# Kernel optimization log

Hardware: AMD Instinct MI355X
Metric: run time of the kernel (lower is better)

The kernel has to match this reference:

```python
import jax, jax.numpy as jnp
import numpy as np

B, T, DIN, E, H, P = 8, 2048, 256, 256, 4, 8
HD = E // H


def _xavier(key, out_dim, in_dim):
    lim = float(np.sqrt(6.0 / (in_dim + out_dim)))
    return jax.random.uniform(key, (out_dim, in_dim), jnp.float32, -lim, lim)


def setup_inputs() -> dict:
    key = jax.random.key(0)
    ks = jax.random.split(key, 9)
    return {
        "x": jax.random.normal(ks[0], (B, T, DIN), jnp.float32),
        "w_in": _xavier(ks[1], E, DIN), "b_in": jnp.zeros((E,), jnp.float32),
        # MHA in-projections (torch packs qkv; xavier over packed [3E,E] approximated per-slice)
        "w_q": _xavier(ks[2], E, E), "b_q": jnp.zeros((E,), jnp.float32),
        "w_k": _xavier(ks[3], E, E), "b_k": jnp.zeros((E,), jnp.float32),
        "w_v": _xavier(ks[4], E, E), "b_v": jnp.zeros((E,), jnp.float32),
        "w_o": _xavier(ks[5], E, E), "b_o": jnp.zeros((E,), jnp.float32),
        "w_bd": _xavier(ks[6], 1, E), "b_bd": jnp.zeros((1,), jnp.float32),
        "w_pr": _xavier(ks[7], E, E), "b_pr": jnp.zeros((E,), jnp.float32),
    }


def reference(x, w_in, b_in, w_q, b_q, w_k, b_k, w_v, b_v, w_o, b_o, w_bd, b_bd, w_pr, b_pr):
    b, t, _ = x.shape
    h = x @ w_in.T + b_in                                   # [B,T,E]
    # self-attention (batch_first MHA, eval mode -> dropout is identity)
    q = (h @ w_q.T + b_q).reshape(b, t, H, HD)
    k = (h @ w_k.T + b_k).reshape(b, t, H, HD)
    v = (h @ w_v.T + b_v).reshape(b, t, H, HD)
    scale = 1.0 / np.sqrt(HD).astype(np.float32)
    scores = jnp.einsum("bqhd,bkhd->bhqk", q * scale, k)   # [B,H,T,T]
    attn = jax.nn.softmax(scores, axis=-1)
    ao = jnp.einsum("bhqk,bkhd->bqhd", attn, v).reshape(b, t, E)
    ao = ao @ w_o.T + b_o
    # boundary scoring -> dynamic patch ids
    bs = jax.nn.sigmoid(ao @ w_bd.T + b_bd)[..., 0]         # [B,T]
    cum = jnp.cumsum(bs, axis=1)
    normalized = cum / jnp.maximum(cum[:, -1:], 1e-6)
    pid = jnp.minimum((normalized * P).astype(jnp.int32), P - 1)  # [B,T]
    # mean-pool h into P dynamic patches (scatter_add + counts, via one-hot segment matmul)
    oh = jax.nn.one_hot(pid, P, dtype=h.dtype)              # [B,T,P]
    patch_emb = jnp.einsum("btp,btd->bpd", oh, h)           # [B,P,E]
    counts = oh.sum(axis=1)[..., None]                      # [B,P,1]
    patch_emb = patch_emb / jnp.maximum(counts, 1.0)
    return patch_emb @ w_pr.T + b_pr                        # [B,P,E]
```

## Files before the change

### kernel.cpp

```cpp
#include <hip/hip_runtime.h>
#include <cstddef>

#define NB 8
#define NT 2048
#define NE 256
#define NH 4
#define ND 64
#define NP 8

typedef short bf16x8 __attribute__((ext_vector_type(8)));
typedef float f32x4 __attribute__((ext_vector_type(4)));
typedef float f32x16 __attribute__((ext_vector_type(16)));

__device__ __forceinline__ unsigned short f2bf(float f) {
  unsigned u = __builtin_bit_cast(unsigned, f);
  u += 0x7fffu + ((u >> 16) & 1u);
  return (unsigned short)(u >> 16);
}
__device__ __forceinline__ float bf2f(unsigned short h) {
  unsigned u = ((unsigned)h) << 16;
  return __builtin_bit_cast(float, u);
}
__device__ __forceinline__ void split2(float a, float b, unsigned& hi, unsigned& lo) {
  const unsigned short ha = f2bf(a), hb = f2bf(b);
  hi = (unsigned)ha | ((unsigned)hb << 16);
  const unsigned short la = f2bf(a - bf2f(ha));
  const unsigned short lb = f2bf(b - bf2f(hb));
  lo = (unsigned)la | ((unsigned)lb << 16);
}
__device__ __forceinline__ void gld16(const void* g, void* l) {
  __builtin_amdgcn_global_load_lds((const __attribute__((address_space(1))) unsigned*)g,
                                   (__attribute__((address_space(3))) unsigned*)l, 16, 0, 0);
}

#define QSC 0.180336880111120419f

__global__ __launch_bounds__(256) void setup1_kernel(
    const float* __restrict__ w_o, const float* __restrict__ b_o,
    const float* __restrict__ w_bd, const float* __restrict__ b_bd,
    const float* __restrict__ w_v, const float* __restrict__ b_v,
    float* __restrict__ uvbuf, float* __restrict__ consts)
{
  __shared__ float wbd_s[NE];
  __shared__ float u_s[NE];
  const int tid = threadIdx.x;
  wbd_s[tid] = w_bd[tid];
  __syncthreads();
  float a = 0.f;
  for (int j = 0; j < NE; ++j) a = fmaf(wbd_s[j], w_o[j * NE + tid], a);
  u_s[tid] = a;
  __syncthreads();
  #pragma unroll
  for (int hh = 0; hh < NH; ++hh) {
    float a2 = 0.f;
    for (int d = 0; d < ND; ++d)
      a2 = fmaf(u_s[hh * ND + d], w_v[(size_t)(hh * ND + d) * NE + tid], a2);
    uvbuf[hh * NE + tid] = a2;
  }
  if (tid == 0) {
    float cc = 0.f;
    for (int j = 0; j < NE; ++j) cc = fmaf(wbd_s[j], b_o[j], cc);
    consts[0] = cc + b_bd[0];
  }
  if (tid >= 8 && tid < 12) {
    const int hh = tid - 8;
    float cv = 0.f;
    for (int d = 0; d < ND; ++d) cv = fmaf(u_s[hh * ND + d], b_v[hh * ND + d], cv);
    consts[1 + hh] = cv;
  }
}

__global__ __launch_bounds__(256) void setup2_kernel(
    const float* __restrict__ w_in, const float* __restrict__ w_q,
    const float* __restrict__ w_k, const float* __restrict__ b_in,
    const float* __restrict__ b_q, const float* __restrict__ b_k,
    const float* __restrict__ uvbuf, const float* __restrict__ consts,
    unsigned short* __restrict__ wfhi, unsigned short* __restrict__ wflo,
    float* __restrict__ bias_f, float* __restrict__ psum)
{
  __shared__ float row_s[256];
  __shared__ float red[256];
  const int b = blockIdx.x, tid = threadIdx.x;
  if (b == 832) {
    for (int i = tid; i < NB * NP * NE; i += 256) psum[i] = 0.f;
    return;
  }
  float v = 0.f, bias = 0.f;
  if (b < 256) {
    v = w_in[(size_t)b * 256 + tid];
    bias = b_in[b];
  } else if (b < 772) {
    const float* wrow = (b < 512) ? (w_q + (size_t)(b - 256) * 256)
                      : (b < 768) ? (w_k + (size_t)(b - 512) * 256)
                                  : (uvbuf + (size_t)(b - 768) * 256);
    row_s[tid] = wrow[tid];
    __syncthreads();
    float acc = 0.f;
    for (int e = 0; e < 256; ++e) acc = fmaf(row_s[e], w_in[(size_t)e * 256 + tid], acc);
    v = acc;
    red[tid] = row_s[tid] * b_in[tid];
    __syncthreads();
    for (int off = 128; off > 0; off >>= 1) {
      if (tid < off) red[tid] += red[tid + off];
      __syncthreads();
    }
    bias = red[0] + ((b < 512) ? b_q[b - 256] : (b < 768) ? b_k[b - 512]
                                              : consts[1 + (b - 768)]);
    if (b < 512) { v *= QSC; bias *= QSC; }
  }
  const unsigned short hb = f2bf(v);
  wfhi[(size_t)b * 256 + tid] = hb;
  wflo[(size_t)b * 256 + tid] = f2bf(v - bf2f(hb));
  if (tid == 0) bias_f[b] = bias;
}

__global__ __launch_bounds__(256) void xgemm_kernel(
    const float* __restrict__ x,
    const unsigned short* __restrict__ wfhi, const unsigned short* __restrict__ wflo,
    const float* __restrict__ bias_f,
    unsigned short* __restrict__ hhi,
    unsigned short* __restrict__ Qhi, unsigned short* __restrict__ Qlo,
    unsigned short* __restrict__ Khi, unsigned short* __restrict__ Klo,
    float* __restrict__ vubuf)
{
  __shared__ __align__(16) char sm[2][24576];
  const int tid = threadIdx.x;
  const int wave = tid >> 6, lane = tid & 63;
  const int lr = lane & 15, lg = lane >> 4;
  const int wm = wave >> 1, wn = wave & 1;
  const int bid = blockIdx.x;
  const int idx = bid >> 3;
  const int m0 = ((bid & 7) * 16 + idx / 13) * 128;
  const int n0 = (idx % 13) * 64;

  const float* aSrc[4];
  #pragma unroll
  for (int c = 0; c < 4; ++c) {
    const int L = c * 4096 + tid * 16;
    const int row = L >> 7, w = (L >> 4) & 7;
    aSrc[c] = x + (size_t)(m0 + row) * 256 + (w ^ (row & 7)) * 4;
  }
  const unsigned short* wSrc[2];
  #pragma unroll
  for (int c = 0; c < 2; ++c) {
    const int L = c * 4096 + tid * 16;
    const int half = (L >> 12) & 1;
    const int Lh = L & 4095;
    const int col = Lh >> 6, w = (Lh >> 4) & 3;
    wSrc[c] = (half ? wflo : wfhi) + (size_t)(n0 + col) * 256 + (w ^ ((col >> 1) & 3)) * 8;
  }
  int aoff[4][2], woff[2];
  #pragma unroll
  for (int s = 0; s < 4; ++s) {
    const int row = wm * 64 + s * 16 + lr;
    const int b0 = row * 128 + lg * 32;
    const int f = (row & 7) << 4;
    aoff[s][0] = b0 ^ f;
    aoff[s][1] = (b0 + 16) ^ f;
  }
  #pragma unroll
  for (int ns = 0; ns < 2; ++ns) {
    const int col = wn * 32 + ns * 16 + lr;
    woff[ns] = (col * 64 + lg * 16) ^ (((col >> 1) & 3) << 4);
  }

  f32x4 acc[4][2];
  #pragma unroll
  for (int s = 0; s < 4; ++s)
    #pragma unroll
    for (int ns = 0; ns < 2; ++ns) acc[s][ns] = (f32x4){0.f, 0.f, 0.f, 0.f};

  {
    char* lb = sm[0];
    #pragma unroll
    for (int c = 0; c < 4; ++c) gld16(aSrc[c], lb + c * 4096 + wave * 1024);
    #pragma unroll
    for (int c = 0; c < 2; ++c) gld16(wSrc[c], lb + 16384 + c * 4096 + wave * 1024);
  }

  for (int kt = 0; kt < 8; ++kt) {
    __syncthreads();
    if (kt < 7) {
      char* nb = sm[(kt + 1) & 1];
      #pragma unroll
      for (int c = 0; c < 4; ++c) gld16(aSrc[c] + (kt + 1) * 32, nb + c * 4096 + wave * 1024);
      #pragma unroll
      for (int c = 0; c < 2; ++c) gld16(wSrc[c] + (kt + 1) * 32, nb + 16384 + c * 4096 + wave * 1024);
    }
    const char* lb = sm[kt & 1];
    bf16x8 ah[4], al[4], wh[2], wl[2];
    #pragma unroll
    for (int s = 0; s < 4; ++s) {
      const f32x4 p0 = *(const f32x4*)(lb + aoff[s][0]);
      const f32x4 p1 = *(const f32x4*)(lb + aoff[s][1]);
      unsigned h0, h1, h2, h3, l0, l1, l2, l3;
      split2(p0[0], p0[1], h0, l0);
      split2(p0[2], p0[3], h1, l1);
      split2(p1[0], p1[1], h2, l2);
      split2(p1[2], p1[3], h3, l3);
      const uint4 hu = make_uint4(h0, h1, h2, h3);
      const uint4 lu = make_uint4(l0, l1, l2, l3);
      ah[s] = __builtin_bit_cast(bf16x8, hu);
      al[s] = __builtin_bit_cast(bf16x8, lu);
    }
    #pragma unroll
    for (int ns = 0; ns < 2; ++ns) {
      wh[ns] = *(const bf16x8*)(lb + 16384 + woff[ns]);
      wl[ns] = *(const bf16x8*)(lb + 20480 + woff[ns]);
    }
    #pragma unroll
    for (int s = 0; s < 4; ++s)
      #pragma unroll
      for (int ns = 0; ns < 2; ++ns) {
        acc[s][ns] = __builtin_amdgcn_mfma_f32_16x16x32_bf16(ah[s], wh[ns], acc[s][ns], 0, 0, 0);
        acc[s][ns] = __builtin_amdgcn_mfma_f32_16x16x32_bf16(ah[s], wl[ns], acc[s][ns], 0, 0, 0);
        acc[s][ns] = __builtin_amdgcn_mfma_f32_16x16x32_bf16(al[s], wh[ns], acc[s][ns], 0, 0, 0);
      }
  }
  #pragma unroll
  for (int s = 0; s < 4; ++s)
    #pragma unroll
    for (int ns = 0; ns < 2; ++ns)
      #pragma unroll
      for (int reg = 0; reg < 4; ++reg) {
        const int row = m0 + wm * 64 + s * 16 + lg * 4 + reg;
        const int col = n0 + wn * 32 + ns * 16 + lr;
        const float v = acc[s][ns][reg] + bias_f[col];
        const int b = row >> 11, t = row & 2047;
        if (col < 256) {
          hhi[(size_t)row * 256 + col] = f2bf(v);
        } else if (col < 768) {
          const int c = (col - 256) & 255;
          const int head = c >> 6, d = c & 63;
          const size_t i2 = (((size_t)(b * NH + head)) * NT + t) * ND + d;
          const unsigned short hb = f2bf(v);
          const unsigned short lb2 = f2bf(v - bf2f(hb));
          if (col < 512) { Qhi[i2] = hb; Qlo[i2] = lb2; }
          else           { Khi[i2] = hb; Klo[i2] = lb2; }
        } else if (col < 772) {
          vubuf[((size_t)(b * NH + (col - 768))) * NT + t] = v;
        }
      }
}

__global__ __launch_bounds__(512, 4) void attn_kernel9(
    const unsigned short* __restrict__ qhi, const unsigned short* __restrict__ qlo,
    const unsigned short* __restrict__ khi, const unsigned short* __restrict__ klo,
    const float* __restrict__ vu, float2* __restrict__ part2)
{
  __shared__ __align__(16) char kbuf[4][16384];
  __shared__ float vu_s[256];
  const int tid = threadIdx.x;
  const int wave = tid >> 6, lane = tid & 63;
  const int lk = lane & 31;
  const int lh = lane >> 5;
  const int bid = blockIdx.x;
  const int idx = bid >> 3;
  const int bh = (bid & 7) * 4 + (idx >> 6);
  const int rem = idx & 63;
  const int qt = rem >> 3, kh = rem & 7;
  const size_t base = (size_t)bh * NT * ND;
  const int qrow0 = qt * 256 + wave * 32;
  const int krow0 = kh * 256;

  if (tid < 256) vu_s[tid] = vu[(size_t)bh * NT + krow0 + tid];

  bf16x8 qf[4][2];
  #pragma unroll
  for (int ds = 0; ds < 4; ++ds) {
    const size_t off = base + (size_t)(qrow0 + lk) * ND + ds * 16 + lh * 8;
    qf[ds][0] = *(const bf16x8*)(qhi + off);
    qf[ds][1] = *(const bf16x8*)(qlo + off);
  }

  const int so = (tid * 16) ^ (((tid >> 3) & 7) << 4);
  int ro[2][4];
  #pragma unroll
  for (int sub = 0; sub < 2; ++sub)
    #pragma unroll
    for (int ds = 0; ds < 4; ++ds)
      ro[sub][ds] = (sub * 32 + lk) * 128 + ((32 * ds + 16 * lh) ^ ((lk & 7) << 4));

  const char* srcH = (const char*)(khi + base + (size_t)krow0 * ND);
  const char* srcL = (const char*)(klo + base + (size_t)krow0 * ND);
  #pragma unroll
  for (int t = 0; t < 4; ++t) {
    gld16(srcH + t * 8192 + so, &kbuf[t][wave * 1024]);
    gld16(srcL + t * 8192 + so, &kbuf[t][8192 + wave * 1024]);
  }
  __syncthreads();

  float l[16], sv[16];
  #pragma unroll
  for (int i = 0; i < 16; ++i) { l[i] = 0.f; sv[i] = 0.f; }
  f32x16 Z;
  #pragma unroll
  for (int i = 0; i < 16; ++i) Z[i] = 0.f;

  #pragma unroll
  for (int it = 0; it < 4; ++it) {
    const int kt = (it + wave) & 3;
    const char* kb = (const char*)kbuf[kt];
    #pragma unroll
    for (int sub = 0; sub < 2; ++sub) {
      const float vuv = vu_s[kt * 64 + sub * 32 + lk];
      f32x16 acc;
      __builtin_amdgcn_s_setprio(1);
      {
        const bf16x8 kh0 = *(const bf16x8*)(kb + ro[sub][0]);
        const bf16x8 kl0 = *(const bf16x8*)(kb + 8192 + ro[sub][0]);
        acc = __builtin_amdgcn_mfma_f32_32x32x16_bf16(qf[0][0], kh0, Z, 0, 0, 0);
        acc = __builtin_amdgcn_mfma_f32_32x32x16_bf16(qf[0][0], kl0, acc, 0, 0, 0);
        acc = __builtin_amdgcn_mfma_f32_32x32x16_bf16(qf[0][1], kh0, acc, 0, 0, 0);
      }
      {
        const bf16x8 kh1 = *(const bf16x8*)(kb + ro[sub][1]);
        const bf16x8 kl1 = *(const bf16x8*)(kb + 8192 + ro[sub][1]);
        acc = __builtin_amdgcn_mfma_f32_32x32x16_bf16(qf[1][0], kh1, acc, 0, 0, 0);
        acc = __builtin_amdgcn_mfma_f32_32x32x16_bf16(qf[1][0], kl1, acc, 0, 0, 0);
        acc = __builtin_amdgcn_mfma_f32_32x32x16_bf16(qf[1][1], kh1, acc, 0, 0, 0);
      }
      {
        const bf16x8 kh2 = *(const bf16x8*)(kb + ro[sub][2]);
        const bf16x8 kl2 = *(const bf16x8*)(kb + 8192 + ro[sub][2]);
        acc = __builtin_amdgcn_mfma_f32_32x32x16_bf16(qf[2][0], kh2, acc, 0, 0, 0);
        acc = __builtin_amdgcn_mfma_f32_32x32x16_bf16(qf[2][0], kl2, acc, 0, 0, 0);
        acc = __builtin_amdgcn_mfma_f32_32x32x16_bf16(qf[2][1], kh2, acc, 0, 0, 0);
      }
      {
        const bf16x8 kh3 = *(const bf16x8*)(kb + ro[sub][3]);
        const bf16x8 kl3 = *(const bf16x8*)(kb + 8192 + ro[sub][3]);
        acc = __builtin_amdgcn_mfma_f32_32x32x16_bf16(qf[3][0], kh3, acc, 0, 0, 0);
        acc = __builtin_amdgcn_mfma_f32_32x32x16_bf16(qf[3][0], kl3, acc, 0, 0, 0);
        acc = __builtin_amdgcn_mfma_f32_32x32x16_bf16(qf[3][1], kh3, acc, 0, 0, 0);
      }
      __builtin_amdgcn_s_setprio(0);
      #pragma unroll
      for (int reg = 0; reg < 16; ++reg) {
        const float e = __builtin_amdgcn_exp2f(acc[reg]);
        l[reg] += e;
        sv[reg] = fmaf(e, vuv, sv[reg]);
      }
    }
  }
  #pragma unroll
  for (int reg = 0; reg < 16; ++reg) {
    #pragma unroll
    for (int off = 1; off < 32; off <<= 1) {
      l[reg]  += __shfl_xor(l[reg],  off);
      sv[reg] += __shfl_xor(sv[reg], off);
    }
  }
  if (lk == 0) {
    #pragma unroll
    for (int reg = 0; reg < 16; ++reg) {
      const int row = qrow0 + (reg & 3) + 8 * (reg >> 2) + 4 * lh;
      part2[(((size_t)bh * NT + row) << 3) + kh] = make_float2(l[reg], sv[reg]);
    }
  }
}

__global__ __launch_bounds__(256) void combine_kernel(
    const float4* __restrict__ part4, const float* __restrict__ consts,
    float* __restrict__ bs)
{
  const int gid = blockIdx.x * 256 + threadIdx.x;
  const int b = gid >> 11, t = gid & 2047;
  float logit = consts[0];
  #pragma unroll
  for (int hh = 0; hh < NH; ++hh) {
    const size_t p0 = ((size_t)((b * NH + hh) * NT) + t) * 4;
    float lsum = 0.f, ssum = 0.f;
    #pragma unroll
    for (int q = 0; q < 4; ++q) {
      const float4 p = part4[p0 + q];
      lsum += p.x + p.z;
      ssum += p.y + p.w;
    }
    logit += ssum / lsum;
  }
  bs[gid] = 1.f / (1.f + expf(-logit));
}

__global__ __launch_bounds__(256) void boundary_kernel(
    const float* __restrict__ bs, int* __restrict__ pid, int* __restrict__ counts)
{
  const int b = blockIdx.x, tid = threadIdx.x;
  __shared__ float partial[256];
  __shared__ int cnt_s[8];
  float v[8];
  float run = 0.f;
  const float4 b0 = *(const float4*)(bs + b * NT + tid * 8);
  const float4 b1 = *(const float4*)(bs + b * NT + tid * 8 + 4);
  const float bv[8] = {b0.x, b0.y, b0.z, b0.w, b1.x, b1.y, b1.z, b1.w};
  #pragma unroll
  for (int i = 0; i < 8; ++i) { run += bv[i]; v[i] = run; }
  float x = run;
  partial[tid] = x;
  __syncthreads();
  for (int off = 1; off < 256; off <<= 1) {
    const float y = (tid >= off) ? partial[tid - off] : 0.f;
    __syncthreads();
    x += y;
    partial[tid] = x;
    __syncthreads();
  }
  const float total = partial[255];
  if (tid < 8) cnt_s[tid] = 0;
  __syncthreads();
  const float denom = fmaxf(total, 1e-6f);
  const float excl = x - run;
  #pragma unroll
  for (int i = 0; i < 8; ++i) {
    const float norm = (excl + v[i]) / denom;
    int pp = (int)(norm * 8.f);
    pp = pp > 7 ? 7 : pp;
    pid[b * NT + tid * 8 + i] = pp;
    atomicAdd(&cnt_s[pp], 1);
  }
  __syncthreads();
  if (tid < 8) counts[b * 8 + tid] = cnt_s[tid];
}

__global__ __launch_bounds__(256) void pool_kernel(
    const unsigned short* __restrict__ hhi, const int* __restrict__ pid,
    float* __restrict__ psum)
{
  const int b = blockIdx.x >> 4, chunk = blockIdx.x & 15;
  const int tid = threadIdx.x;
  __shared__ int pid_s[128];
  const int t0 = chunk * 128;
  if (tid < 128) pid_s[tid] = pid[b * NT + t0 + tid];
  __syncthreads();
  float acc[8] = {};
  for (int tok = 0; tok < 128; ++tok) {
    const float val = bf2f(hhi[((size_t)b * NT + t0 + tok) * NE + tid]);
    const int p = pid_s[tok];
    #pragma unroll
    for (int pp = 0; pp < 8; ++pp) acc[pp] += (p == pp) ? val : 0.f;
  }
  #pragma unroll
  for (int pp = 0; pp < 8; ++pp)
    atomicAdd(&psum[((size_t)b * NP + pp) * NE + tid], acc[pp]);
}

__global__ __launch_bounds__(256) void final_kernel(
    const float* __restrict__ psum, const int* __restrict__ counts,
    const float* __restrict__ w_pr, const float* __restrict__ b_pr, float* __restrict__ out)
{
  const int bp = blockIdx.x;
  const int tid = threadIdx.x;
  __shared__ float pe[NE];
  const float cnt = fmaxf((float)counts[bp], 1.f);
  pe[tid] = psum[(size_t)bp * NE + tid] / cnt;
  __syncthreads();
  float acc = 0.f;
  for (int e = 0; e < NE; ++e) acc = fmaf(pe[e], w_pr[(size_t)tid * NE + e], acc);
  out[(size_t)bp * NE + tid] = acc + b_pr[tid];
}

extern "C" void kernel_launch(void* const* d_in, const int* in_sizes, int n_in,
                              void* d_out, int out_size, void* d_ws, size_t ws_size,
                              hipStream_t stream) {
  (void)in_sizes; (void)n_in; (void)out_size; (void)ws_size;
  const float* x    = (const float*)d_in[0];
  const float* w_in = (const float*)d_in[1];
  const float* b_in = (const float*)d_in[2];
  const float* w_q  = (const float*)d_in[3];
  const float* b_q  = (const float*)d_in[4];
  const float* w_k  = (const float*)d_in[5];
  const float* b_k  = (const float*)d_in[6];
  const float* w_v  = (const float*)d_in[7];
  const float* b_v  = (const float*)d_in[8];
  const float* w_o  = (const float*)d_in[9];
  const float* b_o  = (const float*)d_in[10];
  const float* w_bd = (const float*)d_in[11];
  const float* b_bd = (const float*)d_in[12];
  const float* w_pr = (const float*)d_in[13];
  const float* b_pr = (const float*)d_in[14];
  float* out = (float*)d_out;

  const size_t M = (size_t)NB * NT;
  unsigned short* hhi = (unsigned short*)d_ws;
  unsigned short* qhi = hhi + M * NE;
  unsigned short* qlo = qhi + M * NE;
  unsigned short* khi = qlo + M * NE;
  unsigned short* klo = khi + M * NE;
  unsigned short* wfhi = klo + M * NE;
  unsigned short* wflo = wfhi + 212992;
  float* bias_f = (float*)(wflo + 212992);
  float* uvbuf  = bias_f + 832;
  float* vubuf  = uvbuf + 1024;
  float* part   = vubuf + 65536;
  float* bsbuf  = part + 1048576;
  float* consts = bsbuf + 16384;
  float* psum   = consts + 8;
  int*   pid    = (int*)(psum + 16384);
  int*   counts = pid + 16384;

  setup1_kernel<<<1, 256, 0, stream>>>(w_o, b_o, w_bd, b_bd, w_v, b_v, uvbuf, consts);
  setup2_kernel<<<833, 256, 0, stream>>>(w_in, w_q, w_k, b_in, b_q, b_k,
      uvbuf, consts, wfhi, wflo, bias_f, psum);
  xgemm_kernel<<<1664, 256, 0, stream>>>(x, wfhi, wflo, bias_f,
      hhi, qhi, qlo, khi, klo, vubuf);
  attn_kernel9<<<2048, 512, 0, stream>>>(qhi, qlo, khi, klo, vubuf, (float2*)part);
  combine_kernel<<<64, 256, 0, stream>>>((const float4*)part, consts, bsbuf);
  boundary_kernel<<<8, 256, 0, stream>>>(bsbuf, pid, counts);
  pool_kernel<<<128, 256, 0, stream>>>(hhi, pid, psum);
  final_kernel<<<64, 256, 0, stream>>>(psum, counts, w_pr, b_pr, out);
}
```

Baseline: 181.2 us.

## Switch attention to 16x16x32 MFMA tiles and batch weight-fold setup rows per block

The attention kernel moves from 32x32x16 to 16x16x32 bf16 MFMA tiles. Each wave now computes two 16-row query subtiles against four 16-key subtiles, and the row reductions shrink to 16-lane shuffles. The launch-bounds occupancy hint is dropped. The setup kernel now handles eight weight rows per block, which cuts its grid from 833 to 98 blocks and reuses each w_in load across eight accumulators. The bias tree reduction becomes warp shuffles. This trades a different MFMA shape and register footprint, with possibly lower occupancy, for fewer setup blocks and less redundant global reading.

```diff
diff --git a/kernel.cpp b/kernel.cpp
--- a/kernel.cpp
+++ b/kernel.cpp
@@ -10,7 +10,6 @@
 
 typedef short bf16x8 __attribute__((ext_vector_type(8)));
 typedef float f32x4 __attribute__((ext_vector_type(4)));
-typedef float f32x16 __attribute__((ext_vector_type(16)));
 
 __device__ __forceinline__ unsigned short f2bf(float f) {
   unsigned u = __builtin_bit_cast(unsigned, f);
@@ -78,40 +77,75 @@
     unsigned short* __restrict__ wfhi, unsigned short* __restrict__ wflo,
     float* __restrict__ bias_f, float* __restrict__ psum)
 {
-  __shared__ float row_s[256];
-  __shared__ float red[256];
   const int b = blockIdx.x, tid = threadIdx.x;
-  if (b == 832) {
+  if (b == 97) {
     for (int i = tid; i < NB * NP * NE; i += 256) psum[i] = 0.f;
     return;
   }
-  float v = 0.f, bias = 0.f;
-  if (b < 256) {
-    v = w_in[(size_t)b * 256 + tid];
-    bias = b_in[b];
-  } else if (b < 772) {
-    const float* wrow = (b < 512) ? (w_q + (size_t)(b - 256) * 256)
-                      : (b < 768) ? (w_k + (size_t)(b - 512) * 256)
-                                  : (uvbuf + (size_t)(b - 768) * 256);
-    row_s[tid] = wrow[tid];
-    __syncthreads();
-    float acc = 0.f;
-    for (int e = 0; e < 256; ++e) acc = fmaf(row_s[e], w_in[(size_t)e * 256 + tid], acc);
-    v = acc;
-    red[tid] = row_s[tid] * b_in[tid];
-    __syncthreads();
-    for (int off = 128; off > 0; off >>= 1) {
-      if (tid < off) red[tid] += red[tid + off];
-      __syncthreads();
-    }
-    bias = red[0] + ((b < 512) ? b_q[b - 256] : (b < 768) ? b_k[b - 512]
-                                              : consts[1 + (b - 768)]);
-    if (b < 512) { v *= QSC; bias *= QSC; }
-  }
-  const unsigned short hb = f2bf(v);
-  wfhi[(size_t)b * 256 + tid] = hb;
-  wflo[(size_t)b * 256 + tid] = f2bf(v - bf2f(hb));
-  if (tid == 0) bias_f[b] = bias;
+  if (b < 32) {
+    const int r0 = b * 8;
+    #pragma unroll
+    for (int j = 0; j < 8; ++j) {
+      const int r = r0 + j;
+      const float v = w_in[(size_t)r * 256 + tid];
+      const unsigned short hb = f2bf(v);
+      wfhi[(size_t)r * 256 + tid] = hb;
+      wflo[(size_t)r * 256 + tid] = f2bf(v - bf2f(hb));
+    }
+    if (tid < 8) bias_f[r0 + tid] = b_in[r0 + tid];
+    return;
+  }
+  __shared__ float row8[8][NE];
+  __shared__ float b_in_s[NE];
+  __shared__ float bias_s[8];
+  const int r0 = 256 + (b - 32) * 8;
+  b_in_s[tid] = b_in[tid];
+  #pragma unroll
+  for (int j = 0; j < 8; ++j) {
+    const int r = r0 + j;
+    float w = 0.f;
+    if (r < 512)      w = w_q[(size_t)(r - 256) * 256 + tid];
+    else if (r < 768) w = w_k[(size_t)(r - 512) * 256 + tid];
+    else if (r < 772) w = uvbuf[(size_t)(r - 768) * 256 + tid];
+    row8[j][tid] = w;
+  }
+  __syncthreads();
+  float acc[8] = {};
+  for (int e = 0; e < 256; ++e) {
+    const float wv = w_in[(size_t)e * 256 + tid];
+    #pragma unroll
+    for (int j = 0; j < 8; ++j) acc[j] = fmaf(row8[j][e], wv, acc[j]);
+  }
+  {
+    const int g = tid >> 5, l32 = tid & 31;
+    float p = 0.f;
+    #pragma unroll
+    for (int m = 0; m < 8; ++m) p = fmaf(row8[g][l32 + 32 * m], b_in_s[l32 + 32 * m], p);
+    p += __shfl_xor(p, 1);  p += __shfl_xor(p, 2);  p += __shfl_xor(p, 4);
+    p += __shfl_xor(p, 8);  p += __shfl_xor(p, 16);
+    if (l32 == 0) {
+      const int r = r0 + g;
+      float base = 0.f;
+      if (r < 512)      base = b_q[r - 256];
+      else if (r < 768) base = b_k[r - 512];
+      else if (r < 772) base = consts[1 + (r - 768)];
+      float bia = p + base;
+      if (r < 512) bia *= QSC;
+      bias_s[g] = bia;
+    }
+  }
+  __syncthreads();
+  #pragma unroll
+  for (int j = 0; j < 8; ++j) {
+    const int r = r0 + j;
+    if (r >= 772) break;
+    float v = acc[j];
+    if (r < 512) v *= QSC;
+    const unsigned short hb = f2bf(v);
+    wfhi[(size_t)r * 256 + tid] = hb;
+    wflo[(size_t)r * 256 + tid] = f2bf(v - bf2f(hb));
+  }
+  if (tid < 8 && r0 + tid < 772) bias_f[r0 + tid] = bias_s[tid];
 }
 
 __global__ __launch_bounds__(256) void xgemm_kernel(
@@ -243,7 +277,7 @@
       }
 }
 
-__global__ __launch_bounds__(512, 4) void attn_kernel9(
+__global__ __launch_bounds__(512) void attn_kernel8(
     const unsigned short* __restrict__ qhi, const unsigned short* __restrict__ qlo,
     const unsigned short* __restrict__ khi, const unsigned short* __restrict__ klo,
     const float* __restrict__ vu, float2* __restrict__ part2)
@@ -252,8 +286,7 @@
   __shared__ float vu_s[256];
   const int tid = threadIdx.x;
   const int wave = tid >> 6, lane = tid & 63;
-  const int lk = lane & 31;
-  const int lh = lane >> 5;
+  const int lr = lane & 15, lg = lane >> 4;
   const int bid = blockIdx.x;
   const int idx = bid >> 3;
   const int bh = (bid & 7) * 4 + (idx >> 6);
@@ -265,22 +298,26 @@
 
   if (tid < 256) vu_s[tid] = vu[(size_t)bh * NT + krow0 + tid];
 
-  bf16x8 qf[4][2];
-  #pragma unroll
-  for (int ds = 0; ds < 4; ++ds) {
-    const size_t off = base + (size_t)(qrow0 + lk) * ND + ds * 16 + lh * 8;
-    qf[ds][0] = *(const bf16x8*)(qhi + off);
-    qf[ds][1] = *(const bf16x8*)(qlo + off);
-  }
+  bf16x8 qf[2][2][2];
+  #pragma unroll
+  for (int s = 0; s < 2; ++s)
+    #pragma unroll
+    for (int ds = 0; ds < 2; ++ds) {
+      const size_t off = base + (size_t)(qrow0 + s * 16 + lr) * ND + ds * 32 + lg * 8;
+      qf[s][ds][0] = *(const bf16x8*)(qhi + off);
+      qf[s][ds][1] = *(const bf16x8*)(qlo + off);
+    }
 
   const int so = (tid * 16) ^ (((tid >> 3) & 7) << 4);
-  int ro[2][4];
-  #pragma unroll
-  for (int sub = 0; sub < 2; ++sub)
-    #pragma unroll
-    for (int ds = 0; ds < 4; ++ds)
-      ro[sub][ds] = (sub * 32 + lk) * 128 + ((32 * ds + 16 * lh) ^ ((lk & 7) << 4));
-
+  int ro0[4], ro1[4];
+  #pragma unroll
+  for (int ns = 0; ns < 4; ++ns) {
+    const int r = ns * 16 + lr;
+    const int sw = (r & 7) << 4;
+    const int ob = r * 128 + lg * 16;
+    ro0[ns] = ob ^ sw;
+    ro1[ns] = (ob + 64) ^ sw;
+  }
   const char* srcH = (const char*)(khi + base + (size_t)krow0 * ND);
   const char* srcL = (const char*)(klo + base + (size_t)krow0 * ND);
   #pragma unroll
@@ -290,73 +327,65 @@
   }
   __syncthreads();
 
-  float l[16], sv[16];
-  #pragma unroll
-  for (int i = 0; i < 16; ++i) { l[i] = 0.f; sv[i] = 0.f; }
-  f32x16 Z;
-  #pragma unroll
-  for (int i = 0; i < 16; ++i) Z[i] = 0.f;
+  float l[8], sv[8];
+  #pragma unroll
+  for (int i = 0; i < 8; ++i) { l[i] = 0.f; sv[i] = 0.f; }
+  const f32x4 Z = (f32x4){0.f, 0.f, 0.f, 0.f};
 
   #pragma unroll
   for (int it = 0; it < 4; ++it) {
     const int kt = (it + wave) & 3;
     const char* kb = (const char*)kbuf[kt];
-    #pragma unroll
-    for (int sub = 0; sub < 2; ++sub) {
-      const float vuv = vu_s[kt * 64 + sub * 32 + lk];
-      f32x16 acc;
-      __builtin_amdgcn_s_setprio(1);
-      {
-        const bf16x8 kh0 = *(const bf16x8*)(kb + ro[sub][0]);
-        const bf16x8 kl0 = *(const bf16x8*)(kb + 8192 + ro[sub][0]);
-        acc = __builtin_amdgcn_mfma_f32_32x32x16_bf16(qf[0][0], kh0, Z, 0, 0, 0);
-        acc = __builtin_amdgcn_mfma_f32_32x32x16_bf16(qf[0][0], kl0, acc, 0, 0, 0);
-        acc = __builtin_amdgcn_mfma_f32_32x32x16_bf16(qf[0][1], kh0, acc, 0, 0, 0);
+    f32x4 acc[2][4];
+    float vuv[4];
+    __builtin_amdgcn_s_setprio(1);
+    #pragma unroll
+    for (int ns = 0; ns < 4; ++ns) {
+      const bf16x8 kh0 = *(const bf16x8*)(kb + ro0[ns]);
+      const bf16x8 kh1 = *(const bf16x8*)(kb + ro1[ns]);
+      const bf16x8 kl0 = *(const bf16x8*)(kb + 8192 + ro0[ns]);
+      const bf16x8 kl1 = *(const bf16x8*)(kb + 8192 + ro1[ns]);
+      vuv[ns] = vu_s[kt * 64 + ns * 16 + lr];
+      #pragma unroll
+      for (int s = 0; s < 2; ++s) {
+        acc[s][ns] = __builtin_amdgcn_mfma_f32_16x16x32_bf16(qf[s][0][0], kh0, Z, 0, 0, 0);
+        acc[s][ns] = __builtin_amdgcn_mfma_f32_16x16x32_bf16(qf[s][0][0], kl0, acc[s][ns], 0, 0, 0);
+        acc[s][ns] = __builtin_amdgcn_mfma_f32_16x16x32_bf16(qf[s][0][1], kh0, acc[s][ns], 0, 0, 0);
+        acc[s][ns] = __builtin_amdgcn_mfma_f32_16x16x32_bf16(qf[s][1][0], kh1, acc[s][ns], 0, 0, 0);
+        acc[s][ns] = __builtin_amdgcn_mfma_f32_16x16x32_bf16(qf[s][1][0], kl1, acc[s][ns], 0, 0, 0);
+        acc[s][ns] = __builtin_amdgcn_mfma_f32_16x16x32_bf16(qf[s][1][1], kh1, acc[s][ns], 0, 0, 0);
       }
-      {
-        const bf16x8 kh1 = *(const bf16x8*)(kb + ro[sub][1]);
-        const bf16x8 kl1 = *(const bf16x8*)(kb + 8192 + ro[sub][1]);
-        acc = __builtin_amdgcn_mfma_f32_32x32x16_bf16(qf[1][0], kh1, acc, 0, 0, 0);
-        acc = __builtin_amdgcn_mfma_f32_32x32x16_bf16(qf[1][0], kl1, acc, 0, 0, 0);
-        acc = __builtin_amdgcn_mfma_f32_32x32x16_bf16(qf[1][1], kh1, acc, 0, 0, 0);
+    }
+    __builtin_amdgcn_s_setprio(0);
+    #pragma unroll
+    for (int s = 0; s < 2; ++s)
+      #pragma unroll
+      for (int reg = 0; reg < 4; ++reg) {
+        const int ri = s * 4 + reg;
+        #pragma unroll
+        for (int ns = 0; ns < 4; ++ns) {
+          const float e = __builtin_amdgcn_exp2f(acc[s][ns][reg]);
+          l[ri] += e;
+          sv[ri] = fmaf(e, vuv[ns], sv[ri]);
+        }
       }
-      {
-        const bf16x8 kh2 = *(const bf16x8*)(kb + ro[sub][2]);
-        const bf16x8 kl2 = *(const bf16x8*)(kb + 8192 + ro[sub][2]);
-        acc = __builtin_amdgcn_mfma_f32_32x32x16_bf16(qf[2][0], kh2, acc, 0, 0, 0);
-        acc = __builtin_amdgcn_mfma_f32_32x32x16_bf16(qf[2][0], kl2, acc, 0, 0, 0);
-        acc = __builtin_amdgcn_mfma_f32_32x32x16_bf16(qf[2][1], kh2, acc, 0, 0, 0);
+  }
+  #pragma unroll
+  for (int ri = 0; ri < 8; ++ri) {
+    #pragma unroll
+    for (int off = 1; off < 16; off <<= 1) {
+      l[ri]  += __shfl_xor(l[ri],  off, 16);
+      sv[ri] += __shfl_xor(sv[ri], off, 16);
+    }
+  }
+  if (lr == 0) {
+    #pragma unroll
+    for (int s = 0; s < 2; ++s)
+      #pragma unroll
+      for (int reg = 0; reg < 4; ++reg) {
+        const int row = qrow0 + s * 16 + lg * 4 + reg;
+        part2[(((size_t)bh * NT + row) << 3) + kh] = make_float2(l[s * 4 + reg], sv[s * 4 + reg]);
       }
-      {
-        const bf16x8 kh3 = *(const bf16x8*)(kb + ro[sub][3]);
-        const bf16x8 kl3 = *(const bf16x8*)(kb + 8192 + ro[sub][3]);
-        acc = __builtin_amdgcn_mfma_f32_32x32x16_bf16(qf[3][0], kh3, acc, 0, 0, 0);
-        acc = __builtin_amdgcn_mfma_f32_32x32x16_bf16(qf[3][0], kl3, acc, 0, 0, 0);
-        acc = __builtin_amdgcn_mfma_f32_32x32x16_bf16(qf[3][1], kh3, acc, 0, 0, 0);
-      }
-      __builtin_amdgcn_s_setprio(0);
-      #pragma unroll
-      for (int reg = 0; reg < 16; ++reg) {
-        const float e = __builtin_amdgcn_exp2f(acc[reg]);
-        l[reg] += e;
-        sv[reg] = fmaf(e, vuv, sv[reg]);
-      }
-    }
-  }
-  #pragma unroll
-  for (int reg = 0; reg < 16; ++reg) {
-    #pragma unroll
-    for (int off = 1; off < 32; off <<= 1) {
-      l[reg]  += __shfl_xor(l[reg],  off);
-      sv[reg] += __shfl_xor(sv[reg], off);
-    }
-  }
-  if (lk == 0) {
-    #pragma unroll
-    for (int reg = 0; reg < 16; ++reg) {
-      const int row = qrow0 + (reg & 3) + 8 * (reg >> 2) + 4 * lh;
-      part2[(((size_t)bh * NT + row) << 3) + kh] = make_float2(l[reg], sv[reg]);
-    }
   }
 }
 
@@ -499,11 +528,11 @@
   int*   counts = pid + 16384;
 
   setup1_kernel<<<1, 256, 0, stream>>>(w_o, b_o, w_bd, b_bd, w_v, b_v, uvbuf, consts);
-  setup2_kernel<<<833, 256, 0, stream>>>(w_in, w_q, w_k, b_in, b_q, b_k,
+  setup2_kernel<<<98, 256, 0, stream>>>(w_in, w_q, w_k, b_in, b_q, b_k,
       uvbuf, consts, wfhi, wflo, bias_f, psum);
   xgemm_kernel<<<1664, 256, 0, stream>>>(x, wfhi, wflo, bias_f,
       hhi, qhi, qlo, khi, klo, vubuf);
-  attn_kernel9<<<2048, 512, 0, stream>>>(qhi, qlo, khi, klo, vubuf, (float2*)part);
+  attn_kernel8<<<2048, 512, 0, stream>>>(qhi, qlo, khi, klo, vubuf, (float2*)part);
   combine_kernel<<<64, 256, 0, stream>>>((const float4*)part, consts, bsbuf);
   boundary_kernel<<<8, 256, 0, stream>>>(bsbuf, pid, counts);
   pool_kernel<<<128, 256, 0, stream>>>(hhi, pid, psum);
```

Result: faster. 171.1 us (-5.6%).
